# Kernel optimization log

Measured on AMD Instinct MI355X. Metric: run time of the kernel, lower is better.

## Reference

```python
import jax, jax.numpy as jnp
import numpy as np

N_NODES = 100000
N_EDGES = 3200000
IN_C = 256
OUT_C = 64
NEG_SLOPE = 0.2  # leaky_relu alpha


def setup_inputs() -> dict:
    key = jax.random.key(0)
    k1, k2, k3, k4 = jax.random.split(key, 4)
    x = jax.random.normal(k1, (N_NODES, IN_C), dtype=jnp.float32)
    edge_index = jax.random.randint(k2, (2, N_EDGES), 0, N_NODES, dtype=jnp.int32)
    # xavier-ish scales
    W = jax.random.normal(k3, (OUT_C, IN_C), dtype=jnp.float32) * (1.0 / np.sqrt(IN_C))
    a = jax.random.normal(k4, (2 * OUT_C, 1), dtype=jnp.float32) * 0.1
    return {"x": x, "edge_index": edge_index, "W": W, "a": a, "num_nodes": N_NODES}


def reference(x, edge_index, W, a, num_nodes):
    # eval mode: dropout is identity
    # add self loops
    loop = jnp.arange(num_nodes, dtype=edge_index.dtype)
    row = jnp.concatenate([edge_index[0], loop])  # source nodes (x_j)
    col = jnp.concatenate([edge_index[1], loop])  # destination nodes (x_i)

    h = x @ W.T  # [N, out_c]

    # e = cat([x_i, x_j], 1) @ a  ==  (h @ a_i)[col] + (h @ a_j)[row]
    a_i = a[:OUT_C, 0]
    a_j = a[OUT_C:, 0]
    s_i = h @ a_i  # [N]
    s_j = h @ a_j  # [N]
    e = jax.nn.leaky_relu(s_i[col] + s_j[row], negative_slope=NEG_SLOPE)  # [E+N]

    # segment softmax over destination node (col)
    m = jax.ops.segment_max(e, col, num_segments=num_nodes)  # [N]
    ex = jnp.exp(e - m[col])
    denom = jax.ops.segment_sum(ex, col, num_segments=num_nodes)  # [N]
    alpha = ex / denom[col]  # [E+N]

    # scatter-add aggregation: out[col] += alpha * h[row]
    out = jax.ops.segment_sum(alpha[:, None] * h[row], col, num_segments=num_nodes)
    return out
```

## Files before the change

kernel.cpp:

```cpp
#include <hip/hip_runtime.h>
#include <hip/hip_bf16.h>
#include <cstddef>
#include <cstdint>

#define IN_C 256
#define OUT_C 64
#define NEG_SLOPE 0.2f
#define BKT2 512
#define PCHUNK 4096
#define MAXB 256
#define CAP 18432

typedef __attribute__((ext_vector_type(4))) float f32x4;
typedef __attribute__((ext_vector_type(8))) short s16x8;

__device__ __forceinline__ float lrelu_exp(float t)
{
    t = (t >= 0.f) ? t : NEG_SLOPE * t;
    return __expf(t);
}

__device__ __forceinline__ float bf2f(ushort u)
{
    return __uint_as_float(((uint32_t)u) << 16);
}

__device__ __forceinline__ ushort f2bf(float f)
{
    uint32_t u = __float_as_uint(f);
    u += 0x7fffu + ((u >> 16) & 1u);
    return (ushort)(u >> 16);
}

__device__ __forceinline__ uint32_t pack_bf2(float f0, float f1)
{
    const uint32_t u0 = __float_as_uint(f0) + 0x8000u;
    const uint32_t u1 = __float_as_uint(f1) + 0x8000u;
    return (u1 & 0xffff0000u) | (u0 >> 16);
}

__global__ __launch_bounds__(256) void wconv_kernel(
    const float* __restrict__ W, ushort* __restrict__ wfrag,
    int* __restrict__ cursor, int nb)
{
    if (blockIdx.x == 64) {
        const int i = threadIdx.x;
        if (i < nb) cursor[i] = i * CAP;
        return;
    }
    const int idx = blockIdx.x * 256 + threadIdx.x;
    const int j = idx & 7;
    const int l = (idx >> 3) & 63;
    const int n = (idx >> 9) & 3;
    const int t = idx >> 11;
    const int k   = t * 32 + ((l >> 4) << 3) + j;
    const int col = n * 16 + (l & 15);
    wfrag[idx] = f2bf(W[col * IN_C + k]);
}

__global__ __launch_bounds__(256) void fused_h_mfma(
    const float* __restrict__ x, const ushort* __restrict__ wfrag,
    const float* __restrict__ a, ushort* __restrict__ hb,
    float* __restrict__ s_i, float* __restrict__ s_j, int n_nodes)
{
    __shared__ ushort Bs[32 * 64 * 8];

    const int tid = threadIdx.x;
    for (int i = tid; i < 2048; i += 256)
        ((float4*)Bs)[i] = ((const float4*)wfrag)[i];
    __syncthreads();

    const int lane = tid & 63;
    const int wv   = tid >> 6;
    const int m    = lane & 15;
    const int quad = lane >> 4;

    const int base = blockIdx.x * 64 + wv * 16;
    int row = base + m;
    if (row >= n_nodes) row = n_nodes - 1;

    f32x4 acc0 = {0.f, 0.f, 0.f, 0.f};
    f32x4 acc1 = {0.f, 0.f, 0.f, 0.f};
    f32x4 acc2 = {0.f, 0.f, 0.f, 0.f};
    f32x4 acc3 = {0.f, 0.f, 0.f, 0.f};

    const float* xrow = x + (size_t)row * IN_C + quad * 8;

    #pragma unroll
    for (int t = 0; t < 8; ++t) {
        const float4 xa = *(const float4*)(xrow + t * 32);
        const float4 xb = *(const float4*)(xrow + t * 32 + 4);
        union { s16x8 v; uint32_t u[4]; } af;
        af.u[0] = pack_bf2(xa.x, xa.y);
        af.u[1] = pack_bf2(xa.z, xa.w);
        af.u[2] = pack_bf2(xb.x, xb.y);
        af.u[3] = pack_bf2(xb.z, xb.w);

        const s16x8 b0 = *(const s16x8*)(Bs + ((t * 4 + 0) * 64 + lane) * 8);
        const s16x8 b1 = *(const s16x8*)(Bs + ((t * 4 + 1) * 64 + lane) * 8);
        const s16x8 b2 = *(const s16x8*)(Bs + ((t * 4 + 2) * 64 + lane) * 8);
        const s16x8 b3 = *(const s16x8*)(Bs + ((t * 4 + 3) * 64 + lane) * 8);

        acc0 = __builtin_amdgcn_mfma_f32_16x16x32_bf16(af.v, b0, acc0, 0, 0, 0);
        acc1 = __builtin_amdgcn_mfma_f32_16x16x32_bf16(af.v, b1, acc1, 0, 0, 0);
        acc2 = __builtin_amdgcn_mfma_f32_16x16x32_bf16(af.v, b2, acc2, 0, 0, 0);
        acc3 = __builtin_amdgcn_mfma_f32_16x16x32_bf16(af.v, b3, acc3, 0, 0, 0);
    }

    const int c0 = lane & 15;
    const float ai0 = a[c0],      ai1 = a[c0 + 16], ai2 = a[c0 + 32], ai3 = a[c0 + 48];
    const float aj0 = a[64 + c0], aj1 = a[80 + c0], aj2 = a[96 + c0], aj3 = a[112 + c0];

    #pragma unroll
    for (int r = 0; r < 4; ++r) {
        const int rowr = base + quad * 4 + r;
        float pi = acc0[r] * ai0 + acc1[r] * ai1 + acc2[r] * ai2 + acc3[r] * ai3;
        float pj = acc0[r] * aj0 + acc1[r] * aj1 + acc2[r] * aj2 + acc3[r] * aj3;
        pi += __shfl_xor(pi, 1, 64);  pj += __shfl_xor(pj, 1, 64);
        pi += __shfl_xor(pi, 2, 64);  pj += __shfl_xor(pj, 2, 64);
        pi += __shfl_xor(pi, 4, 64);  pj += __shfl_xor(pj, 4, 64);
        pi += __shfl_xor(pi, 8, 64);  pj += __shfl_xor(pj, 8, 64);
        if (rowr < n_nodes) {
            ushort* hr = hb + (size_t)rowr * OUT_C + c0;
            hr[0]  = f2bf(acc0[r]);
            hr[16] = f2bf(acc1[r]);
            hr[32] = f2bf(acc2[r]);
            hr[48] = f2bf(acc3[r]);
            if (c0 == 0) { s_i[rowr] = pi; s_j[rowr] = pj; }
        }
    }
}

__global__ __launch_bounds__(256) void partition_kernel(
    const int* __restrict__ ei, int* __restrict__ cursor,
    uint32_t* __restrict__ rec, int n_edges, int nb)
{
    __shared__ int      hist[MAXB];
    __shared__ int      lbase[MAXB];
    __shared__ int      gbase[MAXB];
    __shared__ int      lcur[MAXB];
    __shared__ uint32_t srt[PCHUNK];
    __shared__ uint8_t  bmap[PCHUNK];

    const int tid  = threadIdx.x;
    const int base = blockIdx.x * PCHUNK;
    const int lim  = min(PCHUNK, n_edges - base);

    hist[tid] = 0;
    __syncthreads();

    int rA[PCHUNK / 256], cA[PCHUNK / 256];
    #pragma unroll
    for (int k = 0; k < PCHUNK / 256; ++k) {
        const int i = tid + (k << 8);
        if (i < lim) {
            rA[k] = ei[base + i];
            cA[k] = ei[n_edges + base + i];
            atomicAdd(&hist[(uint32_t)cA[k] >> 9], 1);
        }
    }
    __syncthreads();

    const int v = hist[tid];
    lbase[tid] = v;
    __syncthreads();
    for (int off = 1; off < 256; off <<= 1) {
        const int mine  = lbase[tid];
        const int other = (tid >= off) ? lbase[tid - off] : 0;
        __syncthreads();
        lbase[tid] = mine + other;
        __syncthreads();
    }
    const int excl = lbase[tid] - v;
    __syncthreads();
    lbase[tid] = excl;
    lcur[tid]  = excl;
    gbase[tid] = (tid < nb && v > 0) ? atomicAdd(&cursor[tid], v) : 0;
    __syncthreads();

    #pragma unroll
    for (int k = 0; k < PCHUNK / 256; ++k) {
        const int i = tid + (k << 8);
        if (i < lim) {
            const int r = rA[k];
            const int c = cA[k];
            const int b = (uint32_t)c >> 9;
            const int pos = atomicAdd(&lcur[b], 1);
            srt[pos]  = ((uint32_t)r << 9) | (uint32_t)(c & (BKT2 - 1));
            bmap[pos] = (uint8_t)b;
        }
    }
    __syncthreads();

    for (int i = tid; i < lim; i += 256) {
        const int b = bmap[i];
        rec[gbase[b] + (i - lbase[b])] = srt[i];
    }
}

__global__ __launch_bounds__(1024) void refine_kernel(
    uint32_t* __restrict__ rec, const int* __restrict__ cursor,
    int* __restrict__ nodeoff, int n_nodes, int nb)
{
    __shared__ uint32_t recs[CAP];
    __shared__ int hcnt[BKT2];
    __shared__ int lcur[BKT2];
    __shared__ int sscan[BKT2];

    const int b     = blockIdx.x;
    const int tid   = threadIdx.x;
    const int start = b * CAP;
    const int cnt   = min(cursor[b] - start, CAP);

    if (tid < BKT2) hcnt[tid] = 0;
    __syncthreads();

    const int cnt4 = cnt >> 2;
    for (int i = tid; i < cnt4; i += 1024) {
        const uint4 rv4 = ((const uint4*)(rec + start))[i];
        ((uint4*)recs)[i] = rv4;
        atomicAdd(&hcnt[rv4.x & (BKT2 - 1)], 1);
        atomicAdd(&hcnt[rv4.y & (BKT2 - 1)], 1);
        atomicAdd(&hcnt[rv4.z & (BKT2 - 1)], 1);
        atomicAdd(&hcnt[rv4.w & (BKT2 - 1)], 1);
    }
    for (int i = (cnt & ~3) + tid; i < cnt; i += 1024) {
        const uint32_t rv = rec[start + i];
        recs[i] = rv;
        atomicAdd(&hcnt[rv & (BKT2 - 1)], 1);
    }
    __syncthreads();

    if (tid < BKT2) sscan[tid] = hcnt[tid];
    __syncthreads();
    for (int off = 1; off < BKT2; off <<= 1) {
        int mine = 0, other = 0;
        if (tid < BKT2) {
            mine  = sscan[tid];
            other = (tid >= off) ? sscan[tid - off] : 0;
        }
        __syncthreads();
        if (tid < BKT2) sscan[tid] = mine + other;
        __syncthreads();
    }
    if (tid < BKT2) {
        const int myc  = hcnt[tid];
        const int excl = sscan[tid] - myc;
        lcur[tid] = excl;
        const int g = b * BKT2 + tid;
        if (g < n_nodes) nodeoff[g] = start + excl;
    }
    if (b == nb - 1 && tid == 0) nodeoff[n_nodes] = start + cnt;
    __syncthreads();

    for (int i = tid; i < cnt; i += 1024) {
        const uint32_t rv = recs[i];
        const int pos = atomicAdd(&lcur[rv & (BKT2 - 1)], 1);
        rec[start + pos] = rv;
    }
}

__global__ __launch_bounds__(256) void gather_kernel(
    const uint32_t* __restrict__ rec, const ushort* __restrict__ hb,
    const float* __restrict__ s_i, const float* __restrict__ s_j,
    const int* __restrict__ nodeoff, const int* __restrict__ cursor,
    float* __restrict__ out, int n_nodes)
{
    int wid = (int)((blockIdx.x * 256u + threadIdx.x) >> 6);
    wid = __builtin_amdgcn_readfirstlane(wid);
    if (wid >= n_nodes) return;
    const int lane = threadIdx.x & 63;
    const int g    = lane >> 4;
    const int l4   = lane & 15;
    const uint32_t loff = (uint32_t)(l4 << 3);

    const int o = nodeoff[wid];
    int oe;
    if ((wid & (BKT2 - 1)) == BKT2 - 1) {
        const int b = wid >> 9;
        oe = min(cursor[b], b * CAP + CAP);
    } else {
        oe = nodeoff[wid + 1];
    }

    const float si = s_i[wid];
    const char* hbB = (const char*)hb;

    f32x4 acc = {0.f, 0.f, 0.f, 0.f};
    float dsum = 0.f;

    int e = o;
    for (; e + 16 <= oe; e += 16) {
        uint32_t rv[4];
        #pragma unroll
        for (int q = 0; q < 4; ++q) rv[q] = rec[e + q * 4 + g];
        float sj[4]; uint32_t off[4];
        #pragma unroll
        for (int q = 0; q < 4; ++q) {
            sj[q]  = s_j[rv[q] >> 9];
            off[q] = ((rv[q] & 0xFFFFFE00u) >> 2) + loff;
        }
        uint2 hv[4];
        #pragma unroll
        for (int q = 0; q < 4; ++q) hv[q] = *(const uint2*)(hbB + off[q]);
        #pragma unroll
        for (int q = 0; q < 4; ++q) {
            const float ex = lrelu_exp(si + sj[q]);
            acc[0] += ex * __uint_as_float(hv[q].x << 16);
            acc[1] += ex * __uint_as_float(hv[q].x & 0xffff0000u);
            acc[2] += ex * __uint_as_float(hv[q].y << 16);
            acc[3] += ex * __uint_as_float(hv[q].y & 0xffff0000u);
            dsum += ex;
        }
    }
    for (; e + 4 <= oe; e += 4) {
        const uint32_t rv = rec[e + g];
        const float sj = s_j[rv >> 9];
        const uint32_t off = ((rv & 0xFFFFFE00u) >> 2) + loff;
        const uint2 hv = *(const uint2*)(hbB + off);
        const float ex = lrelu_exp(si + sj);
        acc[0] += ex * __uint_as_float(hv.x << 16);
        acc[1] += ex * __uint_as_float(hv.x & 0xffff0000u);
        acc[2] += ex * __uint_as_float(hv.y << 16);
        acc[3] += ex * __uint_as_float(hv.y & 0xffff0000u);
        dsum += ex;
    }
    if (e < oe) {
        const int m = oe - e;
        const uint32_t rv = rec[e + (g < m ? g : m - 1)];
        const float sj = s_j[rv >> 9];
        const uint32_t off = ((rv & 0xFFFFFE00u) >> 2) + loff;
        const uint2 hv = *(const uint2*)(hbB + off);
        const float ex = (g < m) ? lrelu_exp(si + sj) : 0.f;
        acc[0] += ex * __uint_as_float(hv.x << 16);
        acc[1] += ex * __uint_as_float(hv.x & 0xffff0000u);
        acc[2] += ex * __uint_as_float(hv.y << 16);
        acc[3] += ex * __uint_as_float(hv.y & 0xffff0000u);
        dsum += ex;
    }

    #pragma unroll
    for (int k = 0; k < 4; ++k) {
        acc[k] += __shfl_xor(acc[k], 16, 64);
        acc[k] += __shfl_xor(acc[k], 32, 64);
    }
    dsum += __shfl_xor(dsum, 16, 64);
    dsum += __shfl_xor(dsum, 32, 64);

    const float ex0 = lrelu_exp(si + s_j[wid]);
    const uint2 hs = *(const uint2*)(hbB + (size_t)wid * 128 + loff);
    acc[0] += ex0 * __uint_as_float(hs.x << 16);
    acc[1] += ex0 * __uint_as_float(hs.x & 0xffff0000u);
    acc[2] += ex0 * __uint_as_float(hs.y << 16);
    acc[3] += ex0 * __uint_as_float(hs.y & 0xffff0000u);
    dsum += ex0;

    if (g == 0) {
        float4 o4;
        o4.x = acc[0] / dsum;
        o4.y = acc[1] / dsum;
        o4.z = acc[2] / dsum;
        o4.w = acc[3] / dsum;
        *(float4*)(out + (size_t)wid * OUT_C + (l4 << 2)) = o4;
    }
}

extern "C" void kernel_launch(void* const* d_in, const int* in_sizes, int n_in,
                              void* d_out, int out_size, void* d_ws, size_t ws_size,
                              hipStream_t stream)
{
    const float* x  = (const float*)d_in[0];
    const int*   ei = (const int*)d_in[1];
    const float* W  = (const float*)d_in[2];
    const float* a  = (const float*)d_in[3];

    const int N  = in_sizes[0] / IN_C;
    const int E  = in_sizes[1] / 2;
    const int NB = (N + BKT2 - 1) / BKT2;

    float* out = (float*)d_out;

    char* ws = (char*)d_ws;
    ushort* hb      = (ushort*)ws;                ws += (size_t)N * OUT_C * 2;
    float*  s_i     = (float*)ws;                 ws += (size_t)N * 4;
    float*  s_j     = (float*)ws;                 ws += (size_t)N * 4;
    int*    cursor  = (int*)ws;                   ws += (size_t)MAXB * 4;
    int*    nodeoff = (int*)ws;                   ws += (size_t)(N + 1) * 4;
    ws = (char*)(((uintptr_t)ws + 15) & ~(uintptr_t)15);
    ushort* wfrag   = (ushort*)ws;                ws += 32 * 64 * 8 * 2;
    ws = (char*)(((uintptr_t)ws + 15) & ~(uintptr_t)15);
    uint32_t* rec   = (uint32_t*)ws;

    hipLaunchKernelGGL(wconv_kernel, dim3(65), dim3(256), 0, stream,
                       W, wfrag, cursor, NB);
    hipLaunchKernelGGL(fused_h_mfma, dim3((N + 63) / 64), dim3(256), 0, stream,
                       x, wfrag, a, hb, s_i, s_j, N);

    const int pblocks = (E + PCHUNK - 1) / PCHUNK;
    hipLaunchKernelGGL(partition_kernel, dim3(pblocks), dim3(256), 0, stream,
                       ei, cursor, rec, E, NB);

    hipLaunchKernelGGL(refine_kernel, dim3(NB), dim3(1024), 0, stream,
                       rec, cursor, nodeoff, N, NB);

    hipLaunchKernelGGL(gather_kernel, dim3((N + 3) / 4), dim3(256), 0, stream,
                       rec, hb, s_i, s_j, nodeoff, cursor, out, N);
}
```

Measured before the change: 299.3 us.

## Use nontemporal loads/stores, packed f32x2 FMA, and branchless leaky-relu in aggregation

Edge index and record loads, plus the output store, now use nontemporal builtins so streaming data does not displace the reused h and s_j in cache. The accumulators are split into f32x2 vectors so the compiler can emit packed FMA, and leaky-relu becomes a single fmax. The 16-edge loop now has each lane group read four consecutive records instead of strided ones, which changes the load pattern. These changes cut instruction count and cache pollution, but the nontemporal hints may not help when data is already L2-resident.

Measured after the change: 312.6 us. 4.4% more time.

```diff
diff --git a/kernel.cpp b/kernel.cpp
--- a/kernel.cpp
+++ b/kernel.cpp
@@ -12,13 +12,8 @@
 #define CAP 18432
 
 typedef __attribute__((ext_vector_type(4))) float f32x4;
+typedef __attribute__((ext_vector_type(2))) float f32x2;
 typedef __attribute__((ext_vector_type(8))) short s16x8;
-
-__device__ __forceinline__ float lrelu_exp(float t)
-{
-    t = (t >= 0.f) ? t : NEG_SLOPE * t;
-    return __expf(t);
-}
 
 __device__ __forceinline__ float bf2f(ushort u)
 {
@@ -37,6 +32,11 @@
     const uint32_t u0 = __float_as_uint(f0) + 0x8000u;
     const uint32_t u1 = __float_as_uint(f1) + 0x8000u;
     return (u1 & 0xffff0000u) | (u0 >> 16);
+}
+
+__device__ __forceinline__ float lrelu_exp(float t)
+{
+    return __expf(fmaxf(t, NEG_SLOPE * t));
 }
 
 __global__ __launch_bounds__(256) void wconv_kernel(
@@ -154,8 +154,8 @@
     for (int k = 0; k < PCHUNK / 256; ++k) {
         const int i = tid + (k << 8);
         if (i < lim) {
-            rA[k] = ei[base + i];
-            cA[k] = ei[n_edges + base + i];
+            rA[k] = __builtin_nontemporal_load(ei + base + i);
+            cA[k] = __builtin_nontemporal_load(ei + n_edges + base + i);
             atomicAdd(&hist[(uint32_t)cA[k] >> 9], 1);
         }
     }
@@ -286,14 +286,16 @@
     const float si = s_i[wid];
     const char* hbB = (const char*)hb;
 
-    f32x4 acc = {0.f, 0.f, 0.f, 0.f};
+    f32x2 acc01 = {0.f, 0.f};
+    f32x2 acc23 = {0.f, 0.f};
     float dsum = 0.f;
 
     int e = o;
     for (; e + 16 <= oe; e += 16) {
         uint32_t rv[4];
         #pragma unroll
-        for (int q = 0; q < 4; ++q) rv[q] = rec[e + q * 4 + g];
+        for (int q = 0; q < 4; ++q)
+            rv[q] = __builtin_nontemporal_load(rec + e + (g << 2) + q);
         float sj[4]; uint32_t off[4];
         #pragma unroll
         for (int q = 0; q < 4; ++q) {
@@ -305,63 +307,81 @@
         for (int q = 0; q < 4; ++q) hv[q] = *(const uint2*)(hbB + off[q]);
         #pragma unroll
         for (int q = 0; q < 4; ++q) {
-            const float ex = lrelu_exp(si + sj[q]);
-            acc[0] += ex * __uint_as_float(hv[q].x << 16);
-            acc[1] += ex * __uint_as_float(hv[q].x & 0xffff0000u);
-            acc[2] += ex * __uint_as_float(hv[q].y << 16);
-            acc[3] += ex * __uint_as_float(hv[q].y & 0xffff0000u);
+            const float t  = si + sj[q];
+            const float ex = __expf(fmaxf(t, NEG_SLOPE * t));
+            const f32x2 e2 = {ex, ex};
+            f32x2 h01, h23;
+            h01[0] = __uint_as_float(hv[q].x << 16);
+            h01[1] = __uint_as_float(hv[q].x & 0xffff0000u);
+            h23[0] = __uint_as_float(hv[q].y << 16);
+            h23[1] = __uint_as_float(hv[q].y & 0xffff0000u);
+            acc01 += e2 * h01;
+            acc23 += e2 * h23;
             dsum += ex;
         }
     }
     for (; e + 4 <= oe; e += 4) {
-        const uint32_t rv = rec[e + g];
-        const float sj = s_j[rv >> 9];
+        const uint32_t rv = __builtin_nontemporal_load(rec + e + g);
+        const float sjv = s_j[rv >> 9];
         const uint32_t off = ((rv & 0xFFFFFE00u) >> 2) + loff;
         const uint2 hv = *(const uint2*)(hbB + off);
-        const float ex = lrelu_exp(si + sj);
-        acc[0] += ex * __uint_as_float(hv.x << 16);
-        acc[1] += ex * __uint_as_float(hv.x & 0xffff0000u);
-        acc[2] += ex * __uint_as_float(hv.y << 16);
-        acc[3] += ex * __uint_as_float(hv.y & 0xffff0000u);
+        const float t  = si + sjv;
+        const float ex = __expf(fmaxf(t, NEG_SLOPE * t));
+        const f32x2 e2 = {ex, ex};
+        f32x2 h01, h23;
+        h01[0] = __uint_as_float(hv.x << 16);
+        h01[1] = __uint_as_float(hv.x & 0xffff0000u);
+        h23[0] = __uint_as_float(hv.y << 16);
+        h23[1] = __uint_as_float(hv.y & 0xffff0000u);
+        acc01 += e2 * h01;
+        acc23 += e2 * h23;
         dsum += ex;
     }
     if (e < oe) {
         const int m = oe - e;
         const uint32_t rv = rec[e + (g < m ? g : m - 1)];
-        const float sj = s_j[rv >> 9];
+        const float sjv = s_j[rv >> 9];
         const uint32_t off = ((rv & 0xFFFFFE00u) >> 2) + loff;
         const uint2 hv = *(const uint2*)(hbB + off);
-        const float ex = (g < m) ? lrelu_exp(si + sj) : 0.f;
-        acc[0] += ex * __uint_as_float(hv.x << 16);
-        acc[1] += ex * __uint_as_float(hv.x & 0xffff0000u);
-        acc[2] += ex * __uint_as_float(hv.y << 16);
-        acc[3] += ex * __uint_as_float(hv.y & 0xffff0000u);
+        const float t  = si + sjv;
+        const float ex = (g < m) ? __expf(fmaxf(t, NEG_SLOPE * t)) : 0.f;
+        const f32x2 e2 = {ex, ex};
+        f32x2 h01, h23;
+        h01[0] = __uint_as_float(hv.x << 16);
+        h01[1] = __uint_as_float(hv.x & 0xffff0000u);
+        h23[0] = __uint_as_float(hv.y << 16);
+        h23[1] = __uint_as_float(hv.y & 0xffff0000u);
+        acc01 += e2 * h01;
+        acc23 += e2 * h23;
         dsum += ex;
     }
 
     #pragma unroll
-    for (int k = 0; k < 4; ++k) {
-        acc[k] += __shfl_xor(acc[k], 16, 64);
-        acc[k] += __shfl_xor(acc[k], 32, 64);
+    for (int k = 0; k < 2; ++k) {
+        acc01[k] += __shfl_xor(acc01[k], 16, 64);
+        acc01[k] += __shfl_xor(acc01[k], 32, 64);
+        acc23[k] += __shfl_xor(acc23[k], 16, 64);
+        acc23[k] += __shfl_xor(acc23[k], 32, 64);
     }
     dsum += __shfl_xor(dsum, 16, 64);
     dsum += __shfl_xor(dsum, 32, 64);
 
-    const float ex0 = lrelu_exp(si + s_j[wid]);
+    const float t0  = si + s_j[wid];
+    const float ex0 = __expf(fmaxf(t0, NEG_SLOPE * t0));
     const uint2 hs = *(const uint2*)(hbB + (size_t)wid * 128 + loff);
-    acc[0] += ex0 * __uint_as_float(hs.x << 16);
-    acc[1] += ex0 * __uint_as_float(hs.x & 0xffff0000u);
-    acc[2] += ex0 * __uint_as_float(hs.y << 16);
-    acc[3] += ex0 * __uint_as_float(hs.y & 0xffff0000u);
+    acc01[0] += ex0 * __uint_as_float(hs.x << 16);
+    acc01[1] += ex0 * __uint_as_float(hs.x & 0xffff0000u);
+    acc23[0] += ex0 * __uint_as_float(hs.y << 16);
+    acc23[1] += ex0 * __uint_as_float(hs.y & 0xffff0000u);
     dsum += ex0;
 
     if (g == 0) {
-        float4 o4;
-        o4.x = acc[0] / dsum;
-        o4.y = acc[1] / dsum;
-        o4.z = acc[2] / dsum;
-        o4.w = acc[3] / dsum;
-        *(float4*)(out + (size_t)wid * OUT_C + (l4 << 2)) = o4;
+        f32x4 o4;
+        o4[0] = acc01[0] / dsum;
+        o4[1] = acc01[1] / dsum;
+        o4[2] = acc23[0] / dsum;
+        o4[3] = acc23[1] / dsum;
+        __builtin_nontemporal_store(o4, (f32x4*)(out + (size_t)wid * OUT_C + (l4 << 2)));
     }
 }
 
```
